# Performance work log

Measured on AMD Instinct MI355X. Metric: run time of the kernel, lower is better.

## Reference

```python
import jax, jax.numpy as jnp
import numpy as np

N_NODES = 100000
N_EDGES = 1600000
N_FEAT = 128
HIDDEN = 128
N_GRAPHS = 64
N_CLASSES = 10
BN_EPS = 1e-5


def setup_inputs() -> dict:
    key = jax.random.key(0)
    ks = jax.random.split(key, 24)
    glorot = lambda k, o, i: jax.random.normal(k, (o, i), jnp.float32) * (1.0 / np.sqrt(i))
    inp = {
        'x': jax.random.normal(ks[0], (N_NODES, N_FEAT), jnp.float32),
        'edge_index': jax.random.randint(ks[1], (2, N_EDGES), 0, N_NODES, jnp.int64),
        'batch': jnp.sort(jax.random.randint(ks[2], (N_NODES,), 0, N_GRAPHS, jnp.int64)),
        # GCNConv(128 -> 128)
        'gcn_w': glorot(ks[3], HIDDEN, N_FEAT),
        'gcn_b': jnp.zeros((HIDDEN,), jnp.float32),
        # SAGEConv layers 1, 2: lin_l (aggregated, with bias) + lin_r (root, no bias)
        'sage1_wl': glorot(ks[4], HIDDEN, HIDDEN),
        'sage1_bl': jnp.zeros((HIDDEN,), jnp.float32),
        'sage1_wr': glorot(ks[5], HIDDEN, HIDDEN),
        'sage2_wl': glorot(ks[6], HIDDEN, HIDDEN),
        'sage2_bl': jnp.zeros((HIDDEN,), jnp.float32),
        'sage2_wr': glorot(ks[7], HIDDEN, HIDDEN),
        # ClassifierBase: 128 -> 200 -> 100 -> 50 -> 10
        'clf_w0': glorot(ks[8], 200, HIDDEN), 'clf_b0': jnp.zeros((200,), jnp.float32),
        'clf_w1': glorot(ks[9], 100, 200), 'clf_b1': jnp.zeros((100,), jnp.float32),
        'clf_w2': glorot(ks[10], 50, 100), 'clf_b2': jnp.zeros((50,), jnp.float32),
        'clf_w3': glorot(ks[11], N_CLASSES, 50), 'clf_b3': jnp.zeros((N_CLASSES,), jnp.float32),
        # BatchNorm1d (eval mode, running_mean=0, running_var=1)
        'bn0_g': jnp.ones((200,), jnp.float32), 'bn0_b': jnp.zeros((200,), jnp.float32),
        'bn1_g': jnp.ones((100,), jnp.float32), 'bn1_b': jnp.zeros((100,), jnp.float32),
        'bn2_g': jnp.ones((50,), jnp.float32), 'bn2_b': jnp.zeros((50,), jnp.float32),
    }
    return inp


def _gcn_conv(x, src, dst, W, b):
    # PyG GCNConv: add self loops, symmetric deg^{-1/2} normalization
    xw = x @ W.T                                                  # [N, H]
    ones = jnp.ones(src.shape[0], xw.dtype)
    deg = jax.ops.segment_sum(ones, dst, num_segments=N_NODES) + 1.0  # self loops
    dinv = jax.lax.rsqrt(deg)
    norm = dinv[src] * dinv[dst]                                  # [E]
    out = jax.ops.segment_sum(xw[src] * norm[:, None], dst, num_segments=N_NODES)
    out = out + xw * (dinv * dinv)[:, None]                       # self-loop term deg^{-1}
    return out + b


def _sage_conv(x, src, dst, Wl, bl, Wr):
    # PyG SAGEConv (mean aggr): lin_l(mean_{j->i} x_j) + lin_r(x_i)
    ones = jnp.ones(src.shape[0], x.dtype)
    cnt = jax.ops.segment_sum(ones, dst, num_segments=N_NODES)
    agg = jax.ops.segment_sum(x[src], dst, num_segments=N_NODES)
    agg = agg / jnp.maximum(cnt, 1.0)[:, None]
    return agg @ Wl.T + bl + x @ Wr.T


def _bn_eval(h, g, b):
    # eval-mode BatchNorm1d with running_mean=0, running_var=1
    return h * (g / np.sqrt(1.0 + BN_EPS)) + b


def reference(x, edge_index, batch, gcn_w, gcn_b,
              sage1_wl, sage1_bl, sage1_wr, sage2_wl, sage2_bl, sage2_wr,
              clf_w0, clf_b0, clf_w1, clf_b1, clf_w2, clf_b2, clf_w3, clf_b3,
              bn0_g, bn0_b, bn1_g, bn1_b, bn2_g, bn2_b):
    src, dst = edge_index[0], edge_index[1]
    h = _gcn_conv(x, src, dst, gcn_w, gcn_b)          # act_func is None -> no activation
    h = _sage_conv(h, src, dst, sage1_wl, sage1_bl, sage1_wr)
    h = _sage_conv(h, src, dst, sage2_wl, sage2_bl, sage2_wr)
    # global mean pool over graphs
    gcnt = jax.ops.segment_sum(jnp.ones(h.shape[0], h.dtype), batch, num_segments=N_GRAPHS)
    g = jax.ops.segment_sum(h, batch, num_segments=N_GRAPHS) / jnp.maximum(gcnt, 1.0)[:, None]
    # ClassifierBase (eval: dropout inactive), tanh activation
    g = jnp.tanh(_bn_eval(g @ clf_w0.T + clf_b0, bn0_g, bn0_b))
    g = jnp.tanh(_bn_eval(g @ clf_w1.T + clf_b1, bn1_g, bn1_b))
    g = jnp.tanh(_bn_eval(g @ clf_w2.T + clf_b2, bn2_g, bn2_b))
    logits = g @ clf_w3.T + clf_b3
    return jax.nn.softmax(logits, axis=1)             # [B, n_classes]
```

## Files before the change

### kernel.cpp

```cpp
#include <hip/hip_runtime.h>

#define N_NODES 100000
#define N_EDGES 1600000
#define NGRAPH 64
#define NBIN 391
#define EPB 2560
#define NBLK 625
#define CAPB 6144
#define CAPP 8960
#define PSPLIT 8

typedef short s8v __attribute__((ext_vector_type(8)));
typedef float f4v __attribute__((ext_vector_type(4)));
typedef float f2v __attribute__((ext_vector_type(2)));

__device__ __forceinline__ float bflo(unsigned u) { return __uint_as_float(u << 16); }
__device__ __forceinline__ float bfhi(unsigned u) { return __uint_as_float(u & 0xffff0000u); }
__device__ __forceinline__ unsigned short f2bf(float f) {
    unsigned u = __float_as_uint(f);
    u += 0x7fffu + ((u >> 16) & 1u);
    return (unsigned short)(u >> 16);
}
__device__ __forceinline__ float bf2f(unsigned short h) { return __uint_as_float(((unsigned)h) << 16); }
__device__ __forceinline__ unsigned pk(float lo, float hi) {
    return (unsigned)f2bf(lo) | ((unsigned)f2bf(hi) << 16);
}
__device__ __forceinline__ float ldv(const void* p, int i, int f32) {
    return f32 ? ((const float*)p)[i] : bf2f(((const unsigned short*)p)[i]);
}
__device__ __forceinline__ f2v up2(unsigned u) {
    f2v t; t.x = bflo(u); t.y = bfhi(u); return t;
}

__global__ __launch_bounds__(256) void k_setup(const unsigned short* __restrict__ x,
                                               const int* __restrict__ ei,
                                               const int* __restrict__ batch,
                                               int* __restrict__ flags,
                                               int* __restrict__ binCur,
                                               int* __restrict__ gstart,
                                               float* __restrict__ pbuf,
                                               const void* b0, const void* bn0g, const void* bn0b,
                                               const void* b1, const void* bn1g, const void* bn1b,
                                               const void* b2, const void* bn2g, const void* bn2b,
                                               const void* b3) {
    __shared__ int cnt[3];
    int tid = threadIdx.x;
    if (tid < 3) cnt[tid] = 0;
    __syncthreads();
    unsigned short h = x[tid * 37];
    int e = (h >> 7) & 0xFF;
    if (e >= 100 && e <= 150) atomicAdd(&cnt[0], 1);
    if (ei[2 * (tid * 5000) + 1] == 0) atomicAdd(&cnt[1], 1);
    if (batch[2 * (tid * 193) + 1] == 0) atomicAdd(&cnt[2], 1);
    __syncthreads();
    int f = (cnt[0] == 256) ? 0 : 1;
    int b64 = (cnt[2] == 256) ? 1 : 0;
    if (tid == 0) {
        flags[0] = f;
        flags[1] = (cnt[1] == 256) ? 1 : 0;
        flags[2] = b64;
    }
    for (int i = tid; i < NBIN; i += 256) binCur[i] = i * CAPB;
    if (tid <= NGRAPH) {
        int g = tid, lo = 0, hi = N_NODES;
        while (lo < hi) {
            int mid = (lo + hi) >> 1;
            int v = b64 ? batch[2 * mid] : batch[mid];
            if (v < g) lo = mid + 1;
            else hi = mid;
        }
        gstart[g] = lo;
    }
    const float invs = rsqrtf(1.0f + 1e-5f);
    if (tid < 200) {
        float a = ldv(bn0g, tid, f) * invs;
        pbuf[tid] = a;
        pbuf[200 + tid] = ldv(b0, tid, f) * a + ldv(bn0b, tid, f);
    }
    if (tid < 100) {
        float a = ldv(bn1g, tid, f) * invs;
        pbuf[400 + tid] = a;
        pbuf[500 + tid] = ldv(b1, tid, f) * a + ldv(bn1b, tid, f);
    }
    if (tid < 50) {
        float a = ldv(bn2g, tid, f) * invs;
        pbuf[600 + tid] = a;
        pbuf[650 + tid] = ldv(b2, tid, f) * a + ldv(bn2b, tid, f);
    }
    if (tid < 10) pbuf[700 + tid] = ldv(b3, tid, f);
}

__global__ __launch_bounds__(256) void k_binfill(const int* __restrict__ ei,
                                                 int* __restrict__ binCur,
                                                 unsigned* __restrict__ staging,
                                                 const int* __restrict__ flags) {
    __shared__ int cnt[NBIN];
    __shared__ int lofs[NBIN];
    __shared__ int curL[NBIN];
    __shared__ int basg[NBIN];
    __shared__ int sA[512], sB[512];
    __shared__ int dbuf[EPB];
    __shared__ unsigned ebuf[EPB];
    int tid = threadIdx.x;
    int i64 = flags[1];
    int base = blockIdx.x * EPB;
    for (int i = tid; i < NBIN; i += 256) cnt[i] = 0;
    __syncthreads();
    #pragma unroll
    for (int k = 0; k < EPB / 512; ++k) {
        int e = base + k * 512 + tid * 2;
        int d0, d1;
        if (i64) {
            uint4 v = *(const uint4*)(ei + 2 * (size_t)(N_EDGES + e));
            d0 = (int)v.x; d1 = (int)v.z;
        } else {
            int2 v = *(const int2*)(ei + (size_t)N_EDGES + e);
            d0 = v.x; d1 = v.y;
        }
        int l = k * 512 + tid * 2;
        dbuf[l] = d0; dbuf[l + 1] = d1;
        if ((unsigned)d0 < N_NODES) atomicAdd(&cnt[d0 >> 8], 1);
        if ((unsigned)d1 < N_NODES) atomicAdd(&cnt[d1 >> 8], 1);
    }
    __syncthreads();
    for (int k = tid; k < 512; k += 256) sA[k] = (k < NBIN) ? cnt[k] : 0;
    __syncthreads();
    int* src = sA;
    int* dst = sB;
    for (int off = 1; off < 512; off <<= 1) {
        for (int k = tid; k < 512; k += 256)
            dst[k] = src[k] + ((k >= off) ? src[k - off] : 0);
        __syncthreads();
        int* t = src; src = dst; dst = t;
    }
    for (int i = tid; i < NBIN; i += 256) {
        int excl = src[i] - cnt[i];
        lofs[i] = excl;
        curL[i] = excl;
        basg[i] = cnt[i] ? atomicAdd(&binCur[i], cnt[i]) : 0;
    }
    __syncthreads();
    #pragma unroll
    for (int k = 0; k < EPB / 512; ++k) {
        int e = base + k * 512 + tid * 2;
        int s0, s1;
        if (i64) {
            uint4 v = *(const uint4*)(ei + 2 * (size_t)e);
            s0 = (int)v.x; s1 = (int)v.z;
        } else {
            int2 v = *(const int2*)(ei + (size_t)e);
            s0 = v.x; s1 = v.y;
        }
        int l = k * 512 + tid * 2;
        #pragma unroll
        for (int h = 0; h < 2; ++h) {
            int d = dbuf[l + h];
            int s = h ? s1 : s0;
            if ((unsigned)d < N_NODES) {
                s = min(max(s, 0), N_NODES - 1);
                int p = atomicAdd(&curL[d >> 8], 1);
                ebuf[p] = ((unsigned)(d & 255) << 20) | (unsigned)s;
            }
        }
    }
    __syncthreads();
    int wid = tid >> 6, lane = tid & 63;
    for (int b = wid; b < NBIN; b += 4) {
        int n = cnt[b], lo = lofs[b], go = basg[b];
        int cap = (b + 1) * CAPB;
        for (int l = lane; l < n; l += 64)
            if (go + l < cap) staging[go + l] = ebuf[lo + l];
    }
}

__global__ __launch_bounds__(256) void k_csr(const unsigned* __restrict__ staging,
                                             const int* __restrict__ binCur,
                                             int* __restrict__ rsA, int* __restrict__ reA,
                                             float* __restrict__ dinv,
                                             int* __restrict__ colidx,
                                             const void* __restrict__ x,
                                             const int* __restrict__ flags,
                                             unsigned* __restrict__ yout,
                                             unsigned* __restrict__ padA) {
    __shared__ int deg[256];
    __shared__ int s[256];
    __shared__ int cur[256];
    __shared__ float sdinv[256];
    __shared__ unsigned ebuf[CAPB];
    __shared__ int colbuf[CAPP];
    int b = blockIdx.x, tid = threadIdx.x;
    int n0 = b << 8;
    int nend = min(256, N_NODES - n0);
    int runStart = b * CAPB;
    int outStart = b * CAPP;
    int runLen = min(binCur[b] - runStart, CAPB);
    deg[tid] = 0;
    __syncthreads();
    for (int i = tid; i < runLen; i += 256) {
        unsigned e = staging[runStart + i];
        ebuf[i] = e;
        atomicAdd(&deg[e >> 20], 1);
    }
    for (int i = tid; i < CAPP; i += 256) colbuf[i] = N_NODES;
    __syncthreads();
    int myDeg = deg[tid];
    int pdeg = (myDeg + 31) & ~31;
    s[tid] = pdeg;
    __syncthreads();
    for (int off = 1; off < 256; off <<= 1) {
        int x2 = (tid >= off) ? s[tid - off] : 0;
        __syncthreads();
        s[tid] += x2;
        __syncthreads();
    }
    int incl = s[tid];
    int lrs = incl - pdeg;
    if (tid < nend) {
        rsA[n0 + tid] = outStart + lrs;
        reA[n0 + tid] = outStart + lrs + myDeg;
        float di = rsqrtf((float)myDeg + 1.0f);
        dinv[n0 + tid] = di;
        sdinv[tid] = di;
    }
    cur[tid] = lrs;
    __syncthreads();
    for (int i = tid; i < runLen; i += 256) {
        unsigned e = ebuf[i];
        int p = atomicAdd(&cur[e >> 20], 1);
        if (p < CAPP) colbuf[p] = (int)(e & 0xFFFFF);
    }
    __syncthreads();
    int ptot = min(s[255], CAPP);
    for (int i = tid; i < ptot; i += 256) colidx[outStart + i] = colbuf[i];
    int f32 = flags[0];
    for (int i = tid; i < nend * 64; i += 256) {
        int nd = i >> 6;
        float di = sdinv[nd];
        size_t gid = (size_t)n0 * 64 + i;
        float lo, hi;
        if (f32) {
            float2 u = ((const float2*)x)[gid];
            lo = u.x; hi = u.y;
        } else {
            unsigned u = ((const unsigned*)x)[gid];
            lo = bflo(u); hi = bfhi(u);
        }
        yout[gid] = pk(di * lo, di * hi);
    }
    if (b == 0 && tid < 64) {
        yout[(size_t)N_NODES * 64 + tid] = 0u;
        padA[(size_t)N_NODES * 64 + tid] = 0u;
    }
}

__global__ __launch_bounds__(256) void k_agg(const uint4* __restrict__ xs,
                                             const int* __restrict__ rsA,
                                             const int* __restrict__ reA,
                                             const float* __restrict__ dinv,
                                             unsigned* __restrict__ out, int mode,
                                             const int* __restrict__ col) {
    int lane = threadIdx.x & 63;
    int node = blockIdx.x * 4 + (threadIdx.x >> 6);
    int glane = lane & 15, grp = lane >> 4;
    int rs = rsA[node], re = reA[node];
    int deg = re - rs;
    int pend = rs + ((deg + 31) & ~31);
    f2v a0 = {0.f, 0.f}, a1 = {0.f, 0.f}, a2 = {0.f, 0.f}, a3 = {0.f, 0.f};
    uint4 selfu = make_uint4(0u, 0u, 0u, 0u);
    if (mode == 0) selfu = xs[(unsigned)node * 16u + glane];

    for (int base = rs; base < pend; base += 32) {
        int4 c0 = *(const int4*)(col + base + grp * 4);
        int4 c1 = *(const int4*)(col + base + 16 + grp * 4);
        uint4 u0 = xs[(unsigned)c0.x * 16u + glane];
        uint4 u1 = xs[(unsigned)c0.y * 16u + glane];
        uint4 u2 = xs[(unsigned)c0.z * 16u + glane];
        uint4 u3 = xs[(unsigned)c0.w * 16u + glane];
        uint4 u4 = xs[(unsigned)c1.x * 16u + glane];
        uint4 u5 = xs[(unsigned)c1.y * 16u + glane];
        uint4 u6 = xs[(unsigned)c1.z * 16u + glane];
        uint4 u7 = xs[(unsigned)c1.w * 16u + glane];
        a0 += up2(u0.x); a1 += up2(u0.y); a2 += up2(u0.z); a3 += up2(u0.w);
        a0 += up2(u1.x); a1 += up2(u1.y); a2 += up2(u1.z); a3 += up2(u1.w);
        a0 += up2(u2.x); a1 += up2(u2.y); a2 += up2(u2.z); a3 += up2(u2.w);
        a0 += up2(u3.x); a1 += up2(u3.y); a2 += up2(u3.z); a3 += up2(u3.w);
        a0 += up2(u4.x); a1 += up2(u4.y); a2 += up2(u4.z); a3 += up2(u4.w);
        a0 += up2(u5.x); a1 += up2(u5.y); a2 += up2(u5.z); a3 += up2(u5.w);
        a0 += up2(u6.x); a1 += up2(u6.y); a2 += up2(u6.z); a3 += up2(u6.w);
        a0 += up2(u7.x); a1 += up2(u7.y); a2 += up2(u7.z); a3 += up2(u7.w);
    }
    float r[8] = {a0.x, a0.y, a1.x, a1.y, a2.x, a2.y, a3.x, a3.y};
    #pragma unroll
    for (int i = 0; i < 8; ++i) {
        float v = r[i];
        v += __shfl_xor(v, 16, 64);
        v += __shfl_xor(v, 32, 64);
        r[i] = v;
    }
    if (mode == 0) {
        float di = dinv[node];
        r[0] = di * (r[0] + bflo(selfu.x)); r[1] = di * (r[1] + bfhi(selfu.x));
        r[2] = di * (r[2] + bflo(selfu.y)); r[3] = di * (r[3] + bfhi(selfu.y));
        r[4] = di * (r[4] + bflo(selfu.z)); r[5] = di * (r[5] + bfhi(selfu.z));
        r[6] = di * (r[6] + bflo(selfu.w)); r[7] = di * (r[7] + bfhi(selfu.w));
    } else {
        float s = 1.0f / fmaxf((float)deg, 1.0f);
        #pragma unroll
        for (int i = 0; i < 8; ++i) r[i] *= s;
    }
    if (grp == 0) {
        uint4 o;
        o.x = pk(r[0], r[1]); o.y = pk(r[2], r[3]);
        o.z = pk(r[4], r[5]); o.w = pk(r[6], r[7]);
        *(uint4*)(out + (size_t)node * 64 + glane * 4) = o;
    }
}

template <int DUAL>
__global__ __launch_bounds__(256) void k_gemm(const unsigned short* A0,
                                              const void* __restrict__ W0,
                                              const unsigned short* __restrict__ A1,
                                              const void* __restrict__ W1,
                                              const void* __restrict__ bias,
                                              unsigned short* out,
                                              const int* __restrict__ flags) {
    __shared__ __align__(16) unsigned short As[64][136];
    __shared__ __align__(16) unsigned short Ws[128][136];
    int f32 = flags[0];
    int tid = threadIdx.x;
    int lane = tid & 63;
    int rowbase = blockIdx.x * 64;
    int lr = lane & 15, q = lane >> 4;
    int m0 = (tid >> 6) * 16;

    f4v acc[8];
    #pragma unroll
    for (int t = 0; t < 8; ++t) acc[t] = (f4v){0.f, 0.f, 0.f, 0.f};

    #pragma unroll
    for (int p = 0; p < (DUAL ? 2 : 1); ++p) {
        const unsigned short* Ap = p ? A1 : A0;
        const void* Wp = p ? W1 : W0;
        if (p) __syncthreads();
        #pragma unroll
        for (int it = 0; it < 4; ++it) {
            int chunk = tid + it * 256;
            int r = chunk >> 4, c8 = (chunk & 15) * 8;
            int grow = rowbase + r;
            uint4 v = make_uint4(0u, 0u, 0u, 0u);
            if (grow < N_NODES) v = *(const uint4*)(Ap + (size_t)grow * 128 + c8);
            *(uint4*)&As[r][c8] = v;
        }
        if (!f32) {
            const unsigned short* Wf = (const unsigned short*)Wp;
            #pragma unroll
            for (int it = 0; it < 8; ++it) {
                int chunk = tid + it * 256;
                int r = chunk >> 4, c8 = (chunk & 15) * 8;
                *(uint4*)&Ws[r][c8] = *(const uint4*)(Wf + r * 128 + c8);
            }
        } else {
            const float* Wf = (const float*)Wp;
            #pragma unroll
            for (int it = 0; it < 16; ++it) {
                int chunk = tid + it * 256;
                int r = chunk >> 5, c4 = (chunk & 31) * 4;
                float4 v = *(const float4*)(Wf + r * 128 + c4);
                unsigned lo = (unsigned)f2bf(v.x) | ((unsigned)f2bf(v.y) << 16);
                unsigned hi = (unsigned)f2bf(v.z) | ((unsigned)f2bf(v.w) << 16);
                *(uint2*)&Ws[r][c4] = make_uint2(lo, hi);
            }
        }
        __syncthreads();
        #pragma unroll
        for (int k = 0; k < 4; ++k) {
            s8v a = *(const s8v*)&As[m0 + lr][k * 32 + q * 8];
            #pragma unroll
            for (int t = 0; t < 8; ++t) {
                s8v b = *(const s8v*)&Ws[t * 16 + lr][k * 32 + q * 8];
                acc[t] = __builtin_amdgcn_mfma_f32_16x16x32_bf16(a, b, acc[t], 0, 0, 0);
            }
        }
    }
    #pragma unroll
    for (int t = 0; t < 8; ++t) {
        int o = t * 16 + lr;
        float bv = ldv(bias, o, f32);
        #pragma unroll
        for (int j = 0; j < 4; ++j) {
            int m = rowbase + m0 + q * 4 + j;
            if (m < N_NODES) out[(size_t)m * 128 + o] = f2bf(acc[t][j] + bv);
        }
    }
}

__global__ __launch_bounds__(256) void k_pool2(const unsigned* __restrict__ h,
                                               const int* __restrict__ gstart,
                                               float* __restrict__ ppool) {
    __shared__ float part[4][128];
    int g = blockIdx.x / PSPLIT, sl = blockIdx.x % PSPLIT;
    int wave = threadIdx.x >> 6, lane = threadIdx.x & 63;
    int s0 = gstart[g], s1 = gstart[g + 1];
    int n = s1 - s0;
    int chunk = (n + PSPLIT - 1) / PSPLIT;
    int r0 = s0 + sl * chunk;
    int r1 = min(r0 + chunk, s1);
    float a0 = 0.f, a1 = 0.f;
    for (int r = r0 + wave; r < r1; r += 4) {
        unsigned u = h[(size_t)r * 64 + lane];
        a0 += bflo(u);
        a1 += bfhi(u);
    }
    part[wave][2 * lane] = a0;
    part[wave][2 * lane + 1] = a1;
    __syncthreads();
    int t = threadIdx.x;
    if (t < 128) {
        float s = part[0][t] + part[1][t] + part[2][t] + part[3][t];
        ppool[(size_t)blockIdx.x * 128 + t] = s;
    }
}

__global__ void k_cvt_w(const void* w0, const void* w1, const void* w2, const void* w3,
                        float* __restrict__ wbuf, const int* __restrict__ flags) {
    int f = flags[0];
    int i = blockIdx.x * 256 + threadIdx.x;
    if (i < 25600) wbuf[i] = ldv(w0, i, f);
    else if (i < 45600) wbuf[i] = ldv(w1, i - 25600, f);
    else if (i < 50600) wbuf[i] = ldv(w2, i - 45600, f);
    else if (i < 51100) wbuf[i] = ldv(w3, i - 50600, f);
}

__global__ __launch_bounds__(256) void k_clf(const float* __restrict__ ppool,
                                             const int* __restrict__ gstart,
                                             const float* __restrict__ wbuf,
                                             const float* __restrict__ pbuf,
                                             void* outv, const int* __restrict__ flags) {
    __shared__ float gin[128];
    __shared__ float ha[200];
    __shared__ float hb[100];
    int b = blockIdx.x, t = threadIdx.x;
    if (t < 128) {
        float s = 0.f;
        #pragma unroll
        for (int k = 0; k < PSPLIT; ++k) s += ppool[(size_t)(b * PSPLIT + k) * 128 + t];
        int cnt = gstart[b + 1] - gstart[b];
        gin[t] = s / fmaxf((float)cnt, 1.0f);
    }
    __syncthreads();
    if (t < 200) {
        const float4* wr = (const float4*)(wbuf + t * 128);
        float s = 0.f;
        #pragma unroll
        for (int k = 0; k < 32; ++k) {
            float4 v = wr[k];
            s += v.x * gin[4 * k] + v.y * gin[4 * k + 1] + v.z * gin[4 * k + 2] + v.w * gin[4 * k + 3];
        }
        ha[t] = tanhf(s * pbuf[t] + pbuf[200 + t]);
    }
    __syncthreads();
    if (t < 100) {
        const float4* wr = (const float4*)(wbuf + 25600 + t * 200);
        float s = 0.f;
        #pragma unroll
        for (int k = 0; k < 50; ++k) {
            float4 v = wr[k];
            s += v.x * ha[4 * k] + v.y * ha[4 * k + 1] + v.z * ha[4 * k + 2] + v.w * ha[4 * k + 3];
        }
        hb[t] = tanhf(s * pbuf[400 + t] + pbuf[500 + t]);
    }
    __syncthreads();
    if (t < 50) {
        const float4* wr = (const float4*)(wbuf + 45600 + t * 100);
        float s = 0.f;
        #pragma unroll
        for (int k = 0; k < 25; ++k) {
            float4 v = wr[k];
            s += v.x * hb[4 * k] + v.y * hb[4 * k + 1] + v.z * hb[4 * k + 2] + v.w * hb[4 * k + 3];
        }
        gin[t] = tanhf(s * pbuf[600 + t] + pbuf[650 + t]);
    }
    __syncthreads();
    if (t == 0) {
        int f = flags[0];
        float lg[10];
        float mx = -1e30f;
        #pragma unroll
        for (int c = 0; c < 10; ++c) {
            const float* wr = wbuf + 50600 + c * 50;
            float s = 0.f;
            for (int k = 0; k < 50; ++k) s += wr[k] * gin[k];
            s += pbuf[700 + c];
            lg[c] = s;
            mx = fmaxf(mx, s);
        }
        float sum = 0.f;
        #pragma unroll
        for (int c = 0; c < 10; ++c) {
            lg[c] = __expf(lg[c] - mx);
            sum += lg[c];
        }
        float inv = 1.0f / sum;
        #pragma unroll
        for (int c = 0; c < 10; ++c) {
            float v = lg[c] * inv;
            if (f) ((float*)outv)[b * 10 + c] = v;
            else ((unsigned short*)outv)[b * 10 + c] = f2bf(v);
        }
    }
}

extern "C" void kernel_launch(void* const* d_in, const int* in_sizes, int n_in,
                              void* d_out, int out_size, void* d_ws, size_t ws_size,
                              hipStream_t stream) {
    const unsigned short* x16 = (const unsigned short*)d_in[0];
    const int* ei = (const int*)d_in[1];
    const int* batch = (const int*)d_in[2];

    char* ws = (char*)d_ws;
    size_t off = 0;
    auto alloc = [&](size_t bytes) {
        size_t r = off;
        off = (off + bytes + 255) & ~(size_t)255;
        return r;
    };
    int* flags = (int*)(ws + alloc(256));
    int* rsA = (int*)(ws + alloc((size_t)N_NODES * 4));
    int* reA = (int*)(ws + alloc((size_t)N_NODES * 4));
    int* colidx = (int*)(ws + alloc((size_t)NBIN * CAPP * 4));
    float* dinv = (float*)(ws + alloc((size_t)N_NODES * 4));
    int* binCur = (int*)(ws + alloc(NBIN * 4));
    int* gstart = (int*)(ws + alloc((NGRAPH + 1) * 4));
    float* pbuf = (float*)(ws + alloc(710 * 4));
    float* ppool = (float*)(ws + alloc((size_t)NGRAPH * PSPLIT * 128 * 4));
    float* wbuf = (float*)(ws + alloc(51100 * 4));
    unsigned short* bufA = (unsigned short*)(ws + alloc((size_t)(N_NODES + 1) * 128 * 2));
    unsigned short* bufB = (unsigned short*)(ws + alloc((size_t)(N_NODES + 1) * 128 * 2));
    unsigned* staging = (unsigned*)bufA;

    k_setup<<<1, 256, 0, stream>>>(x16, ei, batch, flags, binCur, gstart, pbuf,
                                   d_in[12], d_in[19], d_in[20],
                                   d_in[14], d_in[21], d_in[22],
                                   d_in[16], d_in[23], d_in[24], d_in[18]);
    k_cvt_w<<<200, 256, 0, stream>>>(d_in[11], d_in[13], d_in[15], d_in[17], wbuf, flags);

    k_binfill<<<NBLK, 256, 0, stream>>>(ei, binCur, staging, flags);
    k_csr<<<NBIN, 256, 0, stream>>>(staging, binCur, rsA, reA, dinv, colidx,
                                    (const void*)x16, flags, (unsigned*)bufB, (unsigned*)bufA);

    k_agg<<<N_NODES / 4, 256, 0, stream>>>((const uint4*)bufB, rsA, reA, dinv,
                                           (unsigned*)bufA, 0, colidx);
    k_gemm<0><<<(N_NODES + 63) / 64, 256, 0, stream>>>(bufA, d_in[3], nullptr, nullptr, d_in[4],
                                                       bufA, flags);
    k_agg<<<N_NODES / 4, 256, 0, stream>>>((const uint4*)bufA, rsA, reA, dinv,
                                           (unsigned*)bufB, 1, colidx);
    k_gemm<1><<<(N_NODES + 63) / 64, 256, 0, stream>>>(bufB, d_in[5], bufA, d_in[7], d_in[6],
                                                       bufB, flags);
    k_agg<<<N_NODES / 4, 256, 0, stream>>>((const uint4*)bufB, rsA, reA, dinv,
                                           (unsigned*)bufA, 1, colidx);
    k_gemm<1><<<(N_NODES + 63) / 64, 256, 0, stream>>>(bufA, d_in[8], bufB, d_in[10], d_in[9],
                                                       bufA, flags);
    k_pool2<<<NGRAPH * PSPLIT, 256, 0, stream>>>((const unsigned*)bufA, gstart, ppool);
    k_clf<<<NGRAPH, 256, 0, stream>>>(ppool, gstart, wbuf, pbuf, d_out, flags);
}
```

Before: 546.6 us.

## Reduce CSR padding to 16, split prescale kernel, linearize binfill scatter

Pads each node's neighbor list to a multiple of 16 instead of 32 and halves the aggregation inner loop, so fewer padded dummy rows are gathered. Moves the dinv prescaling of x out of the CSR build into a separate grid-wide kernel and drops the shared edge buffer from k_csr, reducing its LDS use. k_binfill now loads src and dst in one pass and writes staging with a flat per-edge scatter using a stored bin id. The cost is less memory-level parallelism per aggregation iteration and one extra kernel launch.

```diff
diff --git a/kernel.cpp b/kernel.cpp
--- a/kernel.cpp
+++ b/kernel.cpp
@@ -7,7 +7,7 @@
 #define EPB 2560
 #define NBLK 625
 #define CAPB 6144
-#define CAPP 8960
+#define CAPP 7168
 #define PSPLIT 8
 
 typedef short s8v __attribute__((ext_vector_type(8)));
@@ -99,8 +99,10 @@
     __shared__ int curL[NBIN];
     __shared__ int basg[NBIN];
     __shared__ int sA[512], sB[512];
+    __shared__ int sbuf[EPB];
     __shared__ int dbuf[EPB];
     __shared__ unsigned ebuf[EPB];
+    __shared__ unsigned short bbuf[EPB];
     int tid = threadIdx.x;
     int i64 = flags[1];
     int base = blockIdx.x * EPB;
@@ -109,15 +111,20 @@
     #pragma unroll
     for (int k = 0; k < EPB / 512; ++k) {
         int e = base + k * 512 + tid * 2;
-        int d0, d1;
+        int s0, s1, d0, d1;
         if (i64) {
-            uint4 v = *(const uint4*)(ei + 2 * (size_t)(N_EDGES + e));
-            d0 = (int)v.x; d1 = (int)v.z;
+            uint4 vs = *(const uint4*)(ei + 2 * (size_t)e);
+            uint4 vd = *(const uint4*)(ei + 2 * (size_t)(N_EDGES + e));
+            s0 = (int)vs.x; s1 = (int)vs.z;
+            d0 = (int)vd.x; d1 = (int)vd.z;
         } else {
-            int2 v = *(const int2*)(ei + (size_t)N_EDGES + e);
-            d0 = v.x; d1 = v.y;
+            int2 vs = *(const int2*)(ei + (size_t)e);
+            int2 vd = *(const int2*)(ei + (size_t)N_EDGES + e);
+            s0 = vs.x; s1 = vs.y;
+            d0 = vd.x; d1 = vd.y;
         }
         int l = k * 512 + tid * 2;
+        sbuf[l] = s0; sbuf[l + 1] = s1;
         dbuf[l] = d0; dbuf[l + 1] = d1;
         if ((unsigned)d0 < N_NODES) atomicAdd(&cnt[d0 >> 8], 1);
         if ((unsigned)d1 < N_NODES) atomicAdd(&cnt[d1 >> 8], 1);
@@ -133,6 +140,7 @@
         __syncthreads();
         int* t = src; src = dst; dst = t;
     }
+    int totE = src[NBIN - 1];
     for (int i = tid; i < NBIN; i += 256) {
         int excl = src[i] - cnt[i];
         lofs[i] = excl;
@@ -141,35 +149,22 @@
     }
     __syncthreads();
     #pragma unroll
-    for (int k = 0; k < EPB / 512; ++k) {
-        int e = base + k * 512 + tid * 2;
-        int s0, s1;
-        if (i64) {
-            uint4 v = *(const uint4*)(ei + 2 * (size_t)e);
-            s0 = (int)v.x; s1 = (int)v.z;
-        } else {
-            int2 v = *(const int2*)(ei + (size_t)e);
-            s0 = v.x; s1 = v.y;
-        }
-        int l = k * 512 + tid * 2;
-        #pragma unroll
-        for (int h = 0; h < 2; ++h) {
-            int d = dbuf[l + h];
-            int s = h ? s1 : s0;
-            if ((unsigned)d < N_NODES) {
-                s = min(max(s, 0), N_NODES - 1);
-                int p = atomicAdd(&curL[d >> 8], 1);
-                ebuf[p] = ((unsigned)(d & 255) << 20) | (unsigned)s;
-            }
-        }
-    }
-    __syncthreads();
-    int wid = tid >> 6, lane = tid & 63;
-    for (int b = wid; b < NBIN; b += 4) {
-        int n = cnt[b], lo = lofs[b], go = basg[b];
-        int cap = (b + 1) * CAPB;
-        for (int l = lane; l < n; l += 64)
-            if (go + l < cap) staging[go + l] = ebuf[lo + l];
+    for (int k = 0; k < EPB / 256; ++k) {
+        int l = k * 256 + tid;
+        int d = dbuf[l];
+        int s = sbuf[l];
+        if ((unsigned)d < N_NODES) {
+            s = min(max(s, 0), N_NODES - 1);
+            int p = atomicAdd(&curL[d >> 8], 1);
+            ebuf[p] = ((unsigned)(d & 255) << 20) | (unsigned)s;
+            bbuf[p] = (unsigned short)(d >> 8);
+        }
+    }
+    __syncthreads();
+    for (int i = tid; i < totE; i += 256) {
+        int bb = bbuf[i];
+        int p = basg[bb] + (i - lofs[bb]);
+        if (p < (bb + 1) * CAPB) staging[p] = ebuf[i];
     }
 }
 
@@ -177,16 +172,10 @@
                                              const int* __restrict__ binCur,
                                              int* __restrict__ rsA, int* __restrict__ reA,
                                              float* __restrict__ dinv,
-                                             int* __restrict__ colidx,
-                                             const void* __restrict__ x,
-                                             const int* __restrict__ flags,
-                                             unsigned* __restrict__ yout,
-                                             unsigned* __restrict__ padA) {
+                                             int* __restrict__ colidx) {
     __shared__ int deg[256];
     __shared__ int s[256];
     __shared__ int cur[256];
-    __shared__ float sdinv[256];
-    __shared__ unsigned ebuf[CAPB];
     __shared__ int colbuf[CAPP];
     int b = blockIdx.x, tid = threadIdx.x;
     int n0 = b << 8;
@@ -195,16 +184,13 @@
     int outStart = b * CAPP;
     int runLen = min(binCur[b] - runStart, CAPB);
     deg[tid] = 0;
-    __syncthreads();
-    for (int i = tid; i < runLen; i += 256) {
-        unsigned e = staging[runStart + i];
-        ebuf[i] = e;
-        atomicAdd(&deg[e >> 20], 1);
-    }
     for (int i = tid; i < CAPP; i += 256) colbuf[i] = N_NODES;
     __syncthreads();
+    for (int i = tid; i < runLen; i += 256)
+        atomicAdd(&deg[staging[runStart + i] >> 20], 1);
+    __syncthreads();
     int myDeg = deg[tid];
-    int pdeg = (myDeg + 31) & ~31;
+    int pdeg = (myDeg + 15) & ~15;
     s[tid] = pdeg;
     __syncthreads();
     for (int off = 1; off < 256; off <<= 1) {
@@ -218,39 +204,43 @@
     if (tid < nend) {
         rsA[n0 + tid] = outStart + lrs;
         reA[n0 + tid] = outStart + lrs + myDeg;
-        float di = rsqrtf((float)myDeg + 1.0f);
-        dinv[n0 + tid] = di;
-        sdinv[tid] = di;
+        dinv[n0 + tid] = rsqrtf((float)myDeg + 1.0f);
     }
     cur[tid] = lrs;
     __syncthreads();
     for (int i = tid; i < runLen; i += 256) {
-        unsigned e = ebuf[i];
+        unsigned e = staging[runStart + i];
         int p = atomicAdd(&cur[e >> 20], 1);
         if (p < CAPP) colbuf[p] = (int)(e & 0xFFFFF);
     }
     __syncthreads();
     int ptot = min(s[255], CAPP);
     for (int i = tid; i < ptot; i += 256) colidx[outStart + i] = colbuf[i];
-    int f32 = flags[0];
-    for (int i = tid; i < nend * 64; i += 256) {
-        int nd = i >> 6;
-        float di = sdinv[nd];
-        size_t gid = (size_t)n0 * 64 + i;
-        float lo, hi;
-        if (f32) {
-            float2 u = ((const float2*)x)[gid];
-            lo = u.x; hi = u.y;
-        } else {
-            unsigned u = ((const unsigned*)x)[gid];
-            lo = bflo(u); hi = bfhi(u);
-        }
-        yout[gid] = pk(di * lo, di * hi);
-    }
-    if (b == 0 && tid < 64) {
-        yout[(size_t)N_NODES * 64 + tid] = 0u;
-        padA[(size_t)N_NODES * 64 + tid] = 0u;
-    }
+}
+
+__global__ __launch_bounds__(256) void k_prescale(const void* __restrict__ src,
+                                                  const float* __restrict__ dinv,
+                                                  unsigned* __restrict__ out,
+                                                  unsigned* __restrict__ padA,
+                                                  const int* __restrict__ flags) {
+    int id = blockIdx.x * 256 + threadIdx.x;
+    if (id >= (N_NODES + 1) * 64) return;
+    int node = id >> 6;
+    if (node == N_NODES) {
+        out[id] = 0u;
+        padA[id] = 0u;
+        return;
+    }
+    float di = dinv[node];
+    float lo, hi;
+    if (flags[0]) {
+        float2 u = ((const float2*)src)[id];
+        lo = u.x; hi = u.y;
+    } else {
+        unsigned u = ((const unsigned*)src)[id];
+        lo = bflo(u); hi = bfhi(u);
+    }
+    out[id] = pk(di * lo, di * hi);
 }
 
 __global__ __launch_bounds__(256) void k_agg(const uint4* __restrict__ xs,
@@ -264,30 +254,21 @@
     int glane = lane & 15, grp = lane >> 4;
     int rs = rsA[node], re = reA[node];
     int deg = re - rs;
-    int pend = rs + ((deg + 31) & ~31);
+    int pend = rs + ((deg + 15) & ~15);
     f2v a0 = {0.f, 0.f}, a1 = {0.f, 0.f}, a2 = {0.f, 0.f}, a3 = {0.f, 0.f};
     uint4 selfu = make_uint4(0u, 0u, 0u, 0u);
     if (mode == 0) selfu = xs[(unsigned)node * 16u + glane];
 
-    for (int base = rs; base < pend; base += 32) {
-        int4 c0 = *(const int4*)(col + base + grp * 4);
-        int4 c1 = *(const int4*)(col + base + 16 + grp * 4);
-        uint4 u0 = xs[(unsigned)c0.x * 16u + glane];
-        uint4 u1 = xs[(unsigned)c0.y * 16u + glane];
-        uint4 u2 = xs[(unsigned)c0.z * 16u + glane];
-        uint4 u3 = xs[(unsigned)c0.w * 16u + glane];
-        uint4 u4 = xs[(unsigned)c1.x * 16u + glane];
-        uint4 u5 = xs[(unsigned)c1.y * 16u + glane];
-        uint4 u6 = xs[(unsigned)c1.z * 16u + glane];
-        uint4 u7 = xs[(unsigned)c1.w * 16u + glane];
+    for (int base = rs; base < pend; base += 16) {
+        int4 c = *(const int4*)(col + base + grp * 4);
+        uint4 u0 = xs[(unsigned)c.x * 16u + glane];
+        uint4 u1 = xs[(unsigned)c.y * 16u + glane];
+        uint4 u2 = xs[(unsigned)c.z * 16u + glane];
+        uint4 u3 = xs[(unsigned)c.w * 16u + glane];
         a0 += up2(u0.x); a1 += up2(u0.y); a2 += up2(u0.z); a3 += up2(u0.w);
         a0 += up2(u1.x); a1 += up2(u1.y); a2 += up2(u1.z); a3 += up2(u1.w);
         a0 += up2(u2.x); a1 += up2(u2.y); a2 += up2(u2.z); a3 += up2(u2.w);
         a0 += up2(u3.x); a1 += up2(u3.y); a2 += up2(u3.z); a3 += up2(u3.w);
-        a0 += up2(u4.x); a1 += up2(u4.y); a2 += up2(u4.z); a3 += up2(u4.w);
-        a0 += up2(u5.x); a1 += up2(u5.y); a2 += up2(u5.z); a3 += up2(u5.w);
-        a0 += up2(u6.x); a1 += up2(u6.y); a2 += up2(u6.z); a3 += up2(u6.w);
-        a0 += up2(u7.x); a1 += up2(u7.y); a2 += up2(u7.z); a3 += up2(u7.w);
     }
     float r[8] = {a0.x, a0.y, a1.x, a1.y, a2.x, a2.y, a3.x, a3.y};
     #pragma unroll
@@ -545,9 +526,10 @@
     k_cvt_w<<<200, 256, 0, stream>>>(d_in[11], d_in[13], d_in[15], d_in[17], wbuf, flags);
 
     k_binfill<<<NBLK, 256, 0, stream>>>(ei, binCur, staging, flags);
-    k_csr<<<NBIN, 256, 0, stream>>>(staging, binCur, rsA, reA, dinv, colidx,
-                                    (const void*)x16, flags, (unsigned*)bufB, (unsigned*)bufA);
-
+    k_csr<<<NBIN, 256, 0, stream>>>(staging, binCur, rsA, reA, dinv, colidx);
+
+    k_prescale<<<((N_NODES + 1) * 64 + 255) / 256, 256, 0, stream>>>(
+        (const void*)x16, dinv, (unsigned*)bufB, (unsigned*)bufA, flags);
     k_agg<<<N_NODES / 4, 256, 0, stream>>>((const uint4*)bufB, rsA, reA, dinv,
                                            (unsigned*)bufA, 0, colidx);
     k_gemm<0><<<(N_NODES + 63) / 64, 256, 0, stream>>>(bufA, d_in[3], nullptr, nullptr, d_in[4],
```

Measured after the change: 500.2 us. -8.5%, faster.
